# Performance work log

Hardware: AMD Instinct MI355X
Metric: run time of the kernel (lower is better)

## Reference

```python
import jax, jax.numpy as jnp
import numpy as np

B, T, D, HD = 8, 2048, 1024, 64

def setup_inputs() -> dict:
    key = jax.random.key(0)
    k1, k2, k3, k4 = jax.random.split(key, 4)
    x = jax.random.normal(k1, (B, T, D), dtype=jnp.float32)
    Wq = jax.random.normal(k2, (D, HD), dtype=jnp.float32) * (D ** -0.5)
    Wk = jax.random.normal(k3, (D, HD), dtype=jnp.float32) * (D ** -0.5)
    Wv = jax.random.normal(k4, (D, HD), dtype=jnp.float32) * (D ** -0.5)
    return {"x": x, "Wq": Wq, "Wk": Wk, "Wv": Wv}

def reference(x, Wq, Wk, Wv):
    # x: [B,T,D]; projections: [D,HD]
    q = jnp.einsum('btd,dh->bth', x, Wq)
    k = jnp.einsum('btd,dh->bth', x, Wk)
    v = jnp.einsum('btd,dh->bth', x, Wv)
    hd = q.shape[-1]
    scores = jnp.einsum('bth,bsh->bts', q, k) * (hd ** -0.5)  # [B,T,T]
    t = scores.shape[-1]
    causal = jnp.tril(jnp.ones((t, t), dtype=bool))
    scores = jnp.where(causal, scores, -jnp.inf)
    w = jax.nn.softmax(scores, axis=-1)
    # dropout p=0.0 (eval) -> identity
    return jnp.einsum('bts,bsh->bth', w, v)
```

## Files before the change

kernel.cpp:

```cpp
#include <hip/hip_runtime.h>
#include <hip/hip_bf16.h>
#include <stdint.h>

#define NB 8
#define TT 2048
#define DD 1024
#define HDIM 64

typedef __bf16 bf16x8 __attribute__((ext_vector_type(8)));
typedef float f32x4 __attribute__((ext_vector_type(4)));
typedef ushort u16x4 __attribute__((ext_vector_type(4)));

static_assert(sizeof(bf16x8) == 16, "bf16x8 must be 16 bytes");

__device__ inline ushort f2bf_bits(float f) {
    __hip_bfloat16 h = __float2bfloat16(f);
    return *reinterpret_cast<ushort*>(&h);
}
__device__ inline float bfbits2f(ushort u) {
    unsigned v = ((unsigned)u) << 16;
    return __builtin_bit_cast(float, v);
}
__device__ inline bf16x8 ldb8(const ushort* p) {
    return *reinterpret_cast<const bf16x8*>(p);
}

typedef __attribute__((address_space(3))) uint32_t lds_u32;
typedef const __attribute__((address_space(1))) uint32_t glb_u32;
__device__ inline void gl_lds16(const void* g, void* l) {
    __builtin_amdgcn_global_load_lds((glb_u32*)g, (lds_u32*)l, 16, 0, 0);
}

#define WCNT_VM2   0xF72
#define WCNT_VM5   0xF75
#define WCNT_LGKM0 0xC07F

__device__ inline int probe_f32(const ushort* x) {
    int lane = threadIdx.x & 63;
    int wild = 0;
    #pragma unroll
    for (int j = 0; j < 4; ++j) {
        ushort u = x[(lane * 4 + j) * 32];
        int e = (u >> 7) & 0xFF;
        wild += (e >= 0xC0);
    }
    unsigned long long m = __ballot(wild > 0);
    return __popcll(m) > 8;
}

__global__ __launch_bounds__(256) void k_wt(const ushort* __restrict__ x,
                                            const void* __restrict__ Wq,
                                            const void* __restrict__ Wk,
                                            const void* __restrict__ Wv,
                                            ushort* __restrict__ Wt) {
    int f32m = probe_f32(x);
    int idx = blockIdx.x * 256 + threadIdx.x;
    int mat = idx >> 16;
    int rem = idx & 65535;
    int d = rem >> 6;
    int h = rem & 63;
    const void* W = (mat == 0) ? Wq : (mat == 1) ? Wk : Wv;
    float v;
    if (f32m) v = ((const float*)W)[rem];
    else      v = bfbits2f(((const ushort*)W)[rem]);
    if (mat == 0) v *= 0.18033688011112042f;
    int n    = mat * 64 + h;
    int nt   = n >> 4, ncol = n & 15;
    int kk   = d >> 6, ks = (d >> 5) & 1, qd = (d >> 3) & 3, e = d & 7;
    int f    = nt * 2 + ks;
    Wt[((size_t)(kk * 24 + f)) * 512 + (qd * 16 + ncol) * 8 + e] = f2bf_bits(v);
}

template <int F32M>
__device__ inline void proj_body(const void* __restrict__ xv,
                                 const ushort* __restrict__ Wt,
                                 ushort* __restrict__ Qw,
                                 ushort* __restrict__ Kw,
                                 ushort* __restrict__ Vtw,
                                 ushort* Bf, ushort* Afb) {
    int tid  = threadIdx.x;
    int w    = tid >> 6;
    int lane = tid & 63;
    int quad = lane >> 4;
    int col  = lane & 15;
    int mtw  = w >> 2;
    int nh   = w & 3;
    int m0   = blockIdx.x * 64;

    const float*  xf = (const float*)xv;
    const ushort* xb = (const ushort*)xv;

    auto stageB = [&](int buf, int kkk) {
        int kk24 = (kkk >> 6) * 24;
        #pragma unroll
        for (int j = 0; j < 3; ++j) {
            int f = w * 3 + j;
            gl_lds16(Wt + ((size_t)(kk24 + f)) * 512 + lane * 8,
                     Bf + ((size_t)buf * 24 + f) * 512);
        }
    };

    int arow  = m0 + w * 8 + (lane >> 3);
    int amt_s = w >> 1;
    int colp  = (w & 1) * 8 + (lane >> 3);
    f32x4 arf[2];
    u16x4 arb[2];
    auto loadA = [&](int kkk) {
        #pragma unroll
        for (int i = 0; i < 2; ++i) {
            int c = (lane & 7) + i * 8;
            if (F32M) arf[i] = *reinterpret_cast<const f32x4*>(xf + (size_t)arow * DD + kkk + c * 4);
            else      arb[i] = *reinterpret_cast<const u16x4*>(xb + (size_t)arow * DD + kkk + c * 4);
        }
    };
    auto writeA = [&](int q) {
        #pragma unroll
        for (int i = 0; i < 2; ++i) {
            int c  = (lane & 7) + i * 8;
            int ks = i;
            int qd = (c & 7) >> 1;
            int e0 = (c & 1) * 4;
            u16x4 v;
            if (F32M) {
                #pragma unroll
                for (int j = 0; j < 4; ++j) v[j] = f2bf_bits(arf[i][j]);
            } else {
                v = arb[i];
            }
            *reinterpret_cast<u16x4*>(Afb + ((size_t)q * 16 + amt_s * 2 + ks) * 512
                                      + (qd * 16 + colp) * 8 + e0) = v;
        }
    };

    f32x4 acc[2][3];
    #pragma unroll
    for (int i = 0; i < 2; ++i)
        #pragma unroll
        for (int j = 0; j < 3; ++j) acc[i][j] = (f32x4){0.f, 0.f, 0.f, 0.f};

    loadA(0);
    stageB(0, 0);
    writeA(0);
    __builtin_amdgcn_s_waitcnt(WCNT_LGKM0);

    for (int t = 0; t < 16; ++t) {
        int p   = t & 1;
        int kn1 = (t + 1 < 16) ? (t + 1) * 64 : 960;
        loadA(kn1);
        stageB(p ^ 1, kn1);
        __builtin_amdgcn_s_waitcnt(WCNT_VM5);
        __builtin_amdgcn_s_barrier();

        #pragma unroll
        for (int ks = 0; ks < 2; ++ks) {
            bf16x8 a0 = ldb8(Afb + ((size_t)p * 16 + (mtw * 2 + 0) * 2 + ks) * 512 + lane * 8);
            bf16x8 a1 = ldb8(Afb + ((size_t)p * 16 + (mtw * 2 + 1) * 2 + ks) * 512 + lane * 8);
            #pragma unroll
            for (int j = 0; j < 3; ++j) {
                int nt = nh * 3 + j;
                bf16x8 b = ldb8(Bf + ((size_t)p * 24 + nt * 2 + ks) * 512 + lane * 8);
                acc[0][j] = __builtin_amdgcn_mfma_f32_16x16x32_bf16(a0, b, acc[0][j], 0, 0, 0);
                acc[1][j] = __builtin_amdgcn_mfma_f32_16x16x32_bf16(a1, b, acc[1][j], 0, 0, 0);
            }
        }
        writeA(p ^ 1);
        __builtin_amdgcn_s_waitcnt(WCNT_LGKM0);
        __builtin_amdgcn_s_barrier();
    }

    #pragma unroll
    for (int mloc = 0; mloc < 2; ++mloc) {
        #pragma unroll
        for (int j = 0; j < 3; ++j) {
            int nt  = nh * 3 + j;
            int mat = nt >> 2;
            int h   = (nt & 3) * 16 + col;
            if (mat == 2) {
                #pragma unroll
                for (int r = 0; r < 4; ++r) {
                    int row = m0 + mtw * 32 + mloc * 16 + quad * 4 + r;
                    int bb = row >> 11;
                    int t  = row & (TT - 1);
                    Vtw[(size_t)bb * HDIM * TT + (size_t)h * TT + t] = f2bf_bits(acc[mloc][j][r]);
                }
            } else {
                ushort* outp = (mat == 0) ? Qw : Kw;
                #pragma unroll
                for (int r = 0; r < 4; ++r) {
                    int row = m0 + mtw * 32 + mloc * 16 + quad * 4 + r;
                    outp[(size_t)row * HDIM + h] = f2bf_bits(acc[mloc][j][r]);
                }
            }
        }
    }
}

__global__ __launch_bounds__(512, 4) void k_proj(const void* __restrict__ xv,
                                                 const ushort* __restrict__ Wt,
                                                 ushort* __restrict__ Qw,
                                                 ushort* __restrict__ Kw,
                                                 ushort* __restrict__ Vtw) {
    __shared__ ushort Bf[2 * 24 * 512];
    __shared__ ushort Afb[2 * 16 * 512];
    if (probe_f32((const ushort*)xv)) proj_body<1>(xv, Wt, Qw, Kw, Vtw, Bf, Afb);
    else                              proj_body<0>(xv, Wt, Qw, Kw, Vtw, Bf, Afb);
}

__global__ __launch_bounds__(256) void k_attn(const ushort* __restrict__ Qw,
                                              const ushort* __restrict__ Kw,
                                              const ushort* __restrict__ Vtw,
                                              ushort* __restrict__ Po,
                                              float* __restrict__ Pl) {
    int w    = threadIdx.x >> 6;
    int lane = threadIdx.x & 63;
    int quad = lane >> 4;
    int col  = lane & 15;
    int bid  = blockIdx.x;
    int b    = bid & 7;
    int idx  = 79 - (bid >> 3);
    int c, g;
    if (idx < 32)      { c = 0; g = idx; }
    else if (idx < 56) { c = 1; g = idx - 24; }
    else if (idx < 72) { c = 2; g = idx - 40; }
    else               { c = 3; g = idx - 48; }
    int qb = 4 * g + w;
    int m0 = qb * 16;
    int Bq = (qb < 32) ? qb : (qb < 64) ? 2*qb - 32 : (qb < 96) ? 3*qb - 96 : 4*qb - 192;
    int pid = b * 320 + Bq + c;

    const ushort* Qb = Qw + (size_t)b * TT * HDIM;
    const ushort* Kb = Kw + (size_t)b * TT * HDIM;
    const ushort* Vb = Vtw + (size_t)b * HDIM * TT;

    __shared__ ushort KVb[2][8][512];
    __shared__ __hip_bfloat16 Pls[4][16][40];

    auto stageKV = [&](int buf, int s) {
        #pragma unroll
        for (int j = 0; j < 2; ++j) {
            int f = w * 2 + j;
            const ushort* gp;
            if (f < 4) {
                int half = f & 1;
                int ro   = (f >> 1) * 16;
                gp = Kb + (size_t)(s + ro + col) * HDIM + half * 32 + quad * 8;
            } else {
                int vg = f - 4;
                gp = Vb + (size_t)(vg * 16 + col) * TT + s + quad * 8;
            }
            gl_lds16(gp, &KVb[buf][f][0]);
        }
    };

    bf16x8 qf0 = ldb8(Qb + (size_t)(m0 + col) * HDIM + quad * 8);
    bf16x8 qf1 = ldb8(Qb + (size_t)(m0 + col) * HDIM + 32 + quad * 8);

    f32x4 o0 = {0.f,0.f,0.f,0.f};
    f32x4 o1 = {0.f,0.f,0.f,0.f};
    f32x4 o2 = {0.f,0.f,0.f,0.f};
    f32x4 o3 = {0.f,0.f,0.f,0.f};
    float rsum[4] = {0.f, 0.f, 0.f, 0.f};

    const int start = c * 512;
    const int end   = min(start + 512, 64 * g + 64);

    stageKV(0, start);
    for (int s0 = start; s0 < end; s0 += 32) {
        int p  = ((s0 - start) >> 5) & 1;
        int sn = (s0 + 32 < end) ? s0 + 32 : s0;
        stageKV(p ^ 1, sn);
        __builtin_amdgcn_s_waitcnt(WCNT_VM2);
        __builtin_amdgcn_s_barrier();

        if (s0 < m0 + 16) {
            bf16x8 ck0l = ldb8(&KVb[p][0][lane * 8]);
            bf16x8 ck0h = ldb8(&KVb[p][1][lane * 8]);
            bf16x8 ck1l = ldb8(&KVb[p][2][lane * 8]);
            bf16x8 ck1h = ldb8(&KVb[p][3][lane * 8]);

            f32x4 S0 = {0.f,0.f,0.f,0.f};
            f32x4 S1 = {0.f,0.f,0.f,0.f};
            S0 = __builtin_amdgcn_mfma_f32_16x16x32_bf16(qf0, ck0l, S0, 0, 0, 0);
            S0 = __builtin_amdgcn_mfma_f32_16x16x32_bf16(qf1, ck0h, S0, 0, 0, 0);
            S1 = __builtin_amdgcn_mfma_f32_16x16x32_bf16(qf0, ck1l, S1, 0, 0, 0);
            S1 = __builtin_amdgcn_mfma_f32_16x16x32_bf16(qf1, ck1h, S1, 0, 0, 0);

            #pragma unroll
            for (int r = 0; r < 4; ++r) {
                int trow = m0 + quad * 4 + r;
                float aa = (s0 + col      > trow) ? -1e30f : S0[r];
                float dd = (s0 + 16 + col > trow) ? -1e30f : S1[r];
                float p0 = exp2f(aa);
                float p1 = exp2f(dd);
                rsum[r] += p0 + p1;
                Pls[w][quad * 4 + r][col]      = __float2bfloat16(p0);
                Pls[w][quad * 4 + r][16 + col] = __float2bfloat16(p1);
            }
            bf16x8 pf = *reinterpret_cast<const bf16x8*>(&Pls[w][col][quad * 8]);

            bf16x8 cv0 = ldb8(&KVb[p][4][lane * 8]);
            bf16x8 cv1 = ldb8(&KVb[p][5][lane * 8]);
            bf16x8 cv2 = ldb8(&KVb[p][6][lane * 8]);
            bf16x8 cv3 = ldb8(&KVb[p][7][lane * 8]);
            o0 = __builtin_amdgcn_mfma_f32_16x16x32_bf16(pf, cv0, o0, 0, 0, 0);
            o1 = __builtin_amdgcn_mfma_f32_16x16x32_bf16(pf, cv1, o1, 0, 0, 0);
            o2 = __builtin_amdgcn_mfma_f32_16x16x32_bf16(pf, cv2, o2, 0, 0, 0);
            o3 = __builtin_amdgcn_mfma_f32_16x16x32_bf16(pf, cv3, o3, 0, 0, 0);
        }
        __builtin_amdgcn_s_waitcnt(WCNT_LGKM0);
        __builtin_amdgcn_s_barrier();
    }

    #pragma unroll
    for (int off = 1; off < 16; off <<= 1) {
        #pragma unroll
        for (int r = 0; r < 4; ++r)
            rsum[r] += __shfl_xor(rsum[r], off, 64);
    }

    ushort* pb = Po + (size_t)pid * 1024;
    #pragma unroll
    for (int r = 0; r < 4; ++r) {
        int row = quad * 4 + r;
        pb[row * 64 + 0*16 + col] = f2bf_bits(o0[r]);
        pb[row * 64 + 1*16 + col] = f2bf_bits(o1[r]);
        pb[row * 64 + 2*16 + col] = f2bf_bits(o2[r]);
        pb[row * 64 + 3*16 + col] = f2bf_bits(o3[r]);
        if (col == 0) Pl[pid * 16 + row] = rsum[r];
    }
}

__global__ __launch_bounds__(256) void k_merge(const ushort* __restrict__ x,
                                               const ushort* __restrict__ Po,
                                               const float* __restrict__ Pl,
                                               void* __restrict__ outv) {
    int f32m = probe_f32(x);
    int wid  = blockIdx.x * 4 + (threadIdx.x >> 6);
    int lane = threadIdx.x & 63;
    int row  = lane >> 2;
    int g    = lane & 3;
    int b    = wid >> 7;
    int qb   = wid & 127;
    int nch  = (qb >> 5) + 1;
    int Bq   = (qb < 32) ? qb : (qb < 64) ? 2*qb - 32 : (qb < 96) ? 3*qb - 96 : 4*qb - 192;
    int pid0 = b * 320 + Bq;

    float L = 0.f;
    #pragma unroll
    for (int c = 0; c < 4; ++c)
        if (c < nch) L += Pl[(pid0 + c) * 16 + row];
    float inv = 1.0f / L;

    float o[16];
    #pragma unroll
    for (int j = 0; j < 16; ++j) o[j] = 0.f;
    #pragma unroll
    for (int c = 0; c < 4; ++c) {
        if (c < nch) {
            const ushort* p = Po + (size_t)(pid0 + c) * 1024 + row * 64 + g * 16;
            bf16x8 v0 = ldb8(p);
            bf16x8 v1 = ldb8(p + 8);
            #pragma unroll
            for (int j = 0; j < 8; ++j) {
                o[j]     += (float)v0[j];
                o[8 + j] += (float)v1[j];
            }
        }
    }

    size_t obase = ((size_t)b * TT + qb * 16 + row) * HDIM + g * 16;
    if (f32m) {
        float* ob = (float*)outv + obase;
        #pragma unroll
        for (int j = 0; j < 16; ++j) ob[j] = o[j] * inv;
    } else {
        ushort* ob = (ushort*)outv + obase;
        #pragma unroll
        for (int j = 0; j < 16; ++j) ob[j] = f2bf_bits(o[j] * inv);
    }
}

extern "C" void kernel_launch(void* const* d_in, const int* in_sizes, int n_in,
                              void* d_out, int out_size, void* d_ws, size_t ws_size,
                              hipStream_t stream) {
    const ushort* x = (const ushort*)d_in[0];
    ushort* Wt  = (ushort*)d_ws;
    ushort* Qw  = Wt + 3 * HDIM * DD;
    ushort* Kw  = Qw + (size_t)NB * TT * HDIM;
    ushort* Vtw = Kw + (size_t)NB * TT * HDIM;
    ushort* Po  = Vtw + (size_t)NB * TT * HDIM;
    float*  Pl  = (float*)(Po + (size_t)2560 * 1024);

    k_wt   <<<768, 256, 0, stream>>>(x, d_in[1], d_in[2], d_in[3], Wt);
    k_proj <<<256, 512, 0, stream>>>(d_in[0], Wt, Qw, Kw, Vtw);
    k_attn <<<640, 256, 0, stream>>>(Qw, Kw, Vtw, Po, Pl);
    k_merge<<<256, 256, 0, stream>>>(x, Po, Pl, d_out);
}
```

Baseline: 144.7 us.

## Transpose attention MFMAs to keep P in registers via shuffles instead of LDS

Swaps the MFMA operand order so S and O are computed transposed (keys/head-dim along rows, queries along lanes). P is then repacked into the B-operand layout with cross-lane shuffles, which removes the per-iteration LDS round-trip through the Pls scratch buffer. Each lane now owns a single query row, so the row sum needs only two shuffle steps. Partial outputs are written as 8-byte vector stores. In exchange it adds eight shuffles plus selects per iteration and relies on the transposed layout matching the merge kernel's expectations.

```diff
diff --git a/kernel.cpp b/kernel.cpp
--- a/kernel.cpp
+++ b/kernel.cpp
@@ -10,6 +10,7 @@
 typedef __bf16 bf16x8 __attribute__((ext_vector_type(8)));
 typedef float f32x4 __attribute__((ext_vector_type(4)));
 typedef ushort u16x4 __attribute__((ext_vector_type(4)));
+typedef unsigned int u32x4 __attribute__((ext_vector_type(4)));
 
 static_assert(sizeof(bf16x8) == 16, "bf16x8 must be 16 bytes");
 
@@ -233,7 +234,6 @@
     const ushort* Vb = Vtw + (size_t)b * HDIM * TT;
 
     __shared__ ushort KVb[2][8][512];
-    __shared__ __hip_bfloat16 Pls[4][16][40];
 
     auto stageKV = [&](int buf, int s) {
         #pragma unroll
@@ -259,10 +259,13 @@
     f32x4 o1 = {0.f,0.f,0.f,0.f};
     f32x4 o2 = {0.f,0.f,0.f,0.f};
     f32x4 o3 = {0.f,0.f,0.f,0.f};
-    float rsum[4] = {0.f, 0.f, 0.f, 0.f};
+    float rsum = 0.f;
 
     const int start = c * 512;
     const int end   = min(start + 512, 64 * g + 64);
+    const int qrow  = m0 + col;
+    const int hi    = quad >> 1;
+    const int lowsrc = ((quad & 1) << 5) + col;
 
     stageKV(0, start);
     for (int s0 = start; s0 < end; s0 += 32) {
@@ -280,54 +283,68 @@
 
             f32x4 S0 = {0.f,0.f,0.f,0.f};
             f32x4 S1 = {0.f,0.f,0.f,0.f};
-            S0 = __builtin_amdgcn_mfma_f32_16x16x32_bf16(qf0, ck0l, S0, 0, 0, 0);
-            S0 = __builtin_amdgcn_mfma_f32_16x16x32_bf16(qf1, ck0h, S0, 0, 0, 0);
-            S1 = __builtin_amdgcn_mfma_f32_16x16x32_bf16(qf0, ck1l, S1, 0, 0, 0);
-            S1 = __builtin_amdgcn_mfma_f32_16x16x32_bf16(qf1, ck1h, S1, 0, 0, 0);
-
+            S0 = __builtin_amdgcn_mfma_f32_16x16x32_bf16(ck0l, qf0, S0, 0, 0, 0);
+            S0 = __builtin_amdgcn_mfma_f32_16x16x32_bf16(ck0h, qf1, S0, 0, 0, 0);
+            S1 = __builtin_amdgcn_mfma_f32_16x16x32_bf16(ck1l, qf0, S1, 0, 0, 0);
+            S1 = __builtin_amdgcn_mfma_f32_16x16x32_bf16(ck1h, qf1, S1, 0, 0, 0);
+
+            int kb0 = s0 + quad * 4;
+            float p0[4], p1[4];
             #pragma unroll
             for (int r = 0; r < 4; ++r) {
-                int trow = m0 + quad * 4 + r;
-                float aa = (s0 + col      > trow) ? -1e30f : S0[r];
-                float dd = (s0 + 16 + col > trow) ? -1e30f : S1[r];
-                float p0 = exp2f(aa);
-                float p1 = exp2f(dd);
-                rsum[r] += p0 + p1;
-                Pls[w][quad * 4 + r][col]      = __float2bfloat16(p0);
-                Pls[w][quad * 4 + r][16 + col] = __float2bfloat16(p1);
-            }
-            bf16x8 pf = *reinterpret_cast<const bf16x8*>(&Pls[w][col][quad * 8]);
+                p0[r] = exp2f((kb0 + r      > qrow) ? -1e30f : S0[r]);
+                p1[r] = exp2f((kb0 + 16 + r > qrow) ? -1e30f : S1[r]);
+                rsum += p0[r] + p1[r];
+            }
+            unsigned A0 = (unsigned)f2bf_bits(p0[0]) | ((unsigned)f2bf_bits(p0[1]) << 16);
+            unsigned A1 = (unsigned)f2bf_bits(p0[2]) | ((unsigned)f2bf_bits(p0[3]) << 16);
+            unsigned B0 = (unsigned)f2bf_bits(p1[0]) | ((unsigned)f2bf_bits(p1[1]) << 16);
+            unsigned B1 = (unsigned)f2bf_bits(p1[2]) | ((unsigned)f2bf_bits(p1[3]) << 16);
+
+            int t0, u0;
+            t0 = __shfl((int)A0, lowsrc, 64);      u0 = __shfl((int)B0, lowsrc, 64);
+            unsigned w0 = hi ? (unsigned)u0 : (unsigned)t0;
+            t0 = __shfl((int)A1, lowsrc, 64);      u0 = __shfl((int)B1, lowsrc, 64);
+            unsigned w1 = hi ? (unsigned)u0 : (unsigned)t0;
+            t0 = __shfl((int)A0, lowsrc + 16, 64); u0 = __shfl((int)B0, lowsrc + 16, 64);
+            unsigned w2 = hi ? (unsigned)u0 : (unsigned)t0;
+            t0 = __shfl((int)A1, lowsrc + 16, 64); u0 = __shfl((int)B1, lowsrc + 16, 64);
+            unsigned w3 = hi ? (unsigned)u0 : (unsigned)t0;
+            bf16x8 pf = __builtin_bit_cast(bf16x8, (u32x4){w0, w1, w2, w3});
 
             bf16x8 cv0 = ldb8(&KVb[p][4][lane * 8]);
             bf16x8 cv1 = ldb8(&KVb[p][5][lane * 8]);
             bf16x8 cv2 = ldb8(&KVb[p][6][lane * 8]);
             bf16x8 cv3 = ldb8(&KVb[p][7][lane * 8]);
-            o0 = __builtin_amdgcn_mfma_f32_16x16x32_bf16(pf, cv0, o0, 0, 0, 0);
-            o1 = __builtin_amdgcn_mfma_f32_16x16x32_bf16(pf, cv1, o1, 0, 0, 0);
-            o2 = __builtin_amdgcn_mfma_f32_16x16x32_bf16(pf, cv2, o2, 0, 0, 0);
-            o3 = __builtin_amdgcn_mfma_f32_16x16x32_bf16(pf, cv3, o3, 0, 0, 0);
+            o0 = __builtin_amdgcn_mfma_f32_16x16x32_bf16(cv0, pf, o0, 0, 0, 0);
+            o1 = __builtin_amdgcn_mfma_f32_16x16x32_bf16(cv1, pf, o1, 0, 0, 0);
+            o2 = __builtin_amdgcn_mfma_f32_16x16x32_bf16(cv2, pf, o2, 0, 0, 0);
+            o3 = __builtin_amdgcn_mfma_f32_16x16x32_bf16(cv3, pf, o3, 0, 0, 0);
         }
         __builtin_amdgcn_s_waitcnt(WCNT_LGKM0);
         __builtin_amdgcn_s_barrier();
     }
 
-    #pragma unroll
-    for (int off = 1; off < 16; off <<= 1) {
-        #pragma unroll
-        for (int r = 0; r < 4; ++r)
-            rsum[r] += __shfl_xor(rsum[r], off, 64);
-    }
+    rsum += __shfl_xor(rsum, 16, 64);
+    rsum += __shfl_xor(rsum, 32, 64);
 
     ushort* pb = Po + (size_t)pid * 1024;
-    #pragma unroll
-    for (int r = 0; r < 4; ++r) {
-        int row = quad * 4 + r;
-        pb[row * 64 + 0*16 + col] = f2bf_bits(o0[r]);
-        pb[row * 64 + 1*16 + col] = f2bf_bits(o1[r]);
-        pb[row * 64 + 2*16 + col] = f2bf_bits(o2[r]);
-        pb[row * 64 + 3*16 + col] = f2bf_bits(o3[r]);
-        if (col == 0) Pl[pid * 16 + row] = rsum[r];
-    }
+    {
+        u16x4 v;
+        #pragma unroll
+        for (int r = 0; r < 4; ++r) v[r] = f2bf_bits(o0[r]);
+        *reinterpret_cast<u16x4*>(pb + col * 64 + 0 * 16 + quad * 4) = v;
+        #pragma unroll
+        for (int r = 0; r < 4; ++r) v[r] = f2bf_bits(o1[r]);
+        *reinterpret_cast<u16x4*>(pb + col * 64 + 1 * 16 + quad * 4) = v;
+        #pragma unroll
+        for (int r = 0; r < 4; ++r) v[r] = f2bf_bits(o2[r]);
+        *reinterpret_cast<u16x4*>(pb + col * 64 + 2 * 16 + quad * 4) = v;
+        #pragma unroll
+        for (int r = 0; r < 4; ++r) v[r] = f2bf_bits(o3[r]);
+        *reinterpret_cast<u16x4*>(pb + col * 64 + 3 * 16 + quad * 4) = v;
+    }
+    if (quad == 0) Pl[pid * 16 + col] = rsum;
 }
 
 __global__ __launch_bounds__(256) void k_merge(const ushort* __restrict__ x,
```

Result: no change. 146.8 us (+1.5%).

## Tile V transpose into 32-key blocks and swizzle K/V staging for coalescing

Applied to the files above, without the earlier changes.

The projection kernel now stores V transposed in per-32-key tiles (each tile holding 64 dims by 32 keys contiguously) and writes four consecutive keys per lane as one vector store. The attention kernel stages K and V with fully contiguous row loads into LDS using an XOR swizzle, and reads MFMA fragments through matching swizzled slot functions. The goal is to replace the strided 16-byte global accesses of the old V-transposed layout with contiguous ones and to avoid LDS bank conflicts. The swizzle index math is intricate, so any mismatch between the staging and read mappings would produce wrong results.

```diff
diff --git a/kernel.cpp b/kernel.cpp
--- a/kernel.cpp
+++ b/kernel.cpp
@@ -76,7 +76,7 @@
                                  const ushort* __restrict__ Wt,
                                  ushort* __restrict__ Qw,
                                  ushort* __restrict__ Kw,
-                                 ushort* __restrict__ Vtw,
+                                 ushort* __restrict__ V2,
                                  ushort* Bf, ushort* Afb) {
     int tid  = threadIdx.x;
     int w    = tid >> 6;
@@ -176,13 +176,15 @@
             int mat = nt >> 2;
             int h   = (nt & 3) * 16 + col;
             if (mat == 2) {
+                int row0 = m0 + mtw * 32 + mloc * 16 + quad * 4;
+                int bb   = row0 >> 11;
+                int t0   = row0 & (TT - 1);
+                u16x4 v;
                 #pragma unroll
-                for (int r = 0; r < 4; ++r) {
-                    int row = m0 + mtw * 32 + mloc * 16 + quad * 4 + r;
-                    int bb = row >> 11;
-                    int t  = row & (TT - 1);
-                    Vtw[(size_t)bb * HDIM * TT + (size_t)h * TT + t] = f2bf_bits(acc[mloc][j][r]);
-                }
+                for (int r = 0; r < 4; ++r) v[r] = f2bf_bits(acc[mloc][j][r]);
+                *reinterpret_cast<u16x4*>(V2 + (size_t)bb * HDIM * TT
+                                          + (size_t)(t0 >> 5) * 2048
+                                          + h * 32 + (t0 & 31)) = v;
             } else {
                 ushort* outp = (mat == 0) ? Qw : Kw;
                 #pragma unroll
@@ -199,16 +201,16 @@
                                                  const ushort* __restrict__ Wt,
                                                  ushort* __restrict__ Qw,
                                                  ushort* __restrict__ Kw,
-                                                 ushort* __restrict__ Vtw) {
+                                                 ushort* __restrict__ V2) {
     __shared__ ushort Bf[2 * 24 * 512];
     __shared__ ushort Afb[2 * 16 * 512];
-    if (probe_f32((const ushort*)xv)) proj_body<1>(xv, Wt, Qw, Kw, Vtw, Bf, Afb);
-    else                              proj_body<0>(xv, Wt, Qw, Kw, Vtw, Bf, Afb);
+    if (probe_f32((const ushort*)xv)) proj_body<1>(xv, Wt, Qw, Kw, V2, Bf, Afb);
+    else                              proj_body<0>(xv, Wt, Qw, Kw, V2, Bf, Afb);
 }
 
 __global__ __launch_bounds__(256) void k_attn(const ushort* __restrict__ Qw,
                                               const ushort* __restrict__ Kw,
-                                              const ushort* __restrict__ Vtw,
+                                              const ushort* __restrict__ V2w,
                                               ushort* __restrict__ Po,
                                               float* __restrict__ Pl) {
     int w    = threadIdx.x >> 6;
@@ -228,28 +230,39 @@
     int Bq = (qb < 32) ? qb : (qb < 64) ? 2*qb - 32 : (qb < 96) ? 3*qb - 96 : 4*qb - 192;
     int pid = b * 320 + Bq + c;
 
-    const ushort* Qb = Qw + (size_t)b * TT * HDIM;
-    const ushort* Kb = Kw + (size_t)b * TT * HDIM;
-    const ushort* Vb = Vtw + (size_t)b * HDIM * TT;
-
-    __shared__ ushort KVb[2][8][512];
+    const ushort* Qb  = Qw  + (size_t)b * TT * HDIM;
+    const ushort* Kb  = Kw  + (size_t)b * TT * HDIM;
+    const ushort* V2b = V2w + (size_t)b * HDIM * TT;
+
+    __shared__ ushort KVb[2][4096];
     __shared__ __hip_bfloat16 Pls[4][16][40];
 
     auto stageKV = [&](int buf, int s) {
         #pragma unroll
         for (int j = 0; j < 2; ++j) {
-            int f = w * 2 + j;
+            int i = w * 2 + j;
             const ushort* gp;
-            if (f < 4) {
-                int half = f & 1;
-                int ro   = (f >> 1) * 16;
-                gp = Kb + (size_t)(s + ro + col) * HDIM + half * 32 + quad * 8;
+            if (i < 4) {
+                int row = i * 8 + (lane >> 3);
+                int cg  = (lane & 7) ^ (lane >> 3);
+                gp = Kb + (size_t)(s + row) * HDIM + cg * 8;
             } else {
-                int vg = f - 4;
-                gp = Vb + (size_t)(vg * 16 + col) * TT + s + quad * 8;
-            }
-            gl_lds16(gp, &KVb[buf][f][0]);
-        }
+                int w3 = (lane & 7) ^ (lane >> 3);
+                int d  = (i - 4) * 16 + 2 * (lane >> 3) + (w3 >> 2);
+                int cg = w3 & 3;
+                gp = V2b + (size_t)(s >> 5) * 2048 + d * 32 + cg * 8;
+            }
+            gl_lds16(gp, &KVb[buf][i * 512]);
+        }
+    };
+
+    int cb7  = col & 7;
+    int vlow = (quad + 4 * (col & 1)) ^ ((col >> 1) & 7);
+    auto kslot = [&](int rb, int half) {
+        return ((rb + col) * 8 + ((half * 4 + quad) ^ cb7)) * 8;
+    };
+    auto vslot = [&](int vg) {
+        return 2048 + ((vg * 8 + (col >> 1)) * 8 + vlow) * 8;
     };
 
     bf16x8 qf0 = ldb8(Qb + (size_t)(m0 + col) * HDIM + quad * 8);
@@ -273,10 +286,10 @@
         __builtin_amdgcn_s_barrier();
 
         if (s0 < m0 + 16) {
-            bf16x8 ck0l = ldb8(&KVb[p][0][lane * 8]);
-            bf16x8 ck0h = ldb8(&KVb[p][1][lane * 8]);
-            bf16x8 ck1l = ldb8(&KVb[p][2][lane * 8]);
-            bf16x8 ck1h = ldb8(&KVb[p][3][lane * 8]);
+            bf16x8 ck0l = ldb8(&KVb[p][kslot(0,  0)]);
+            bf16x8 ck0h = ldb8(&KVb[p][kslot(0,  1)]);
+            bf16x8 ck1l = ldb8(&KVb[p][kslot(16, 0)]);
+            bf16x8 ck1h = ldb8(&KVb[p][kslot(16, 1)]);
 
             f32x4 S0 = {0.f,0.f,0.f,0.f};
             f32x4 S1 = {0.f,0.f,0.f,0.f};
@@ -298,10 +311,10 @@
             }
             bf16x8 pf = *reinterpret_cast<const bf16x8*>(&Pls[w][col][quad * 8]);
 
-            bf16x8 cv0 = ldb8(&KVb[p][4][lane * 8]);
-            bf16x8 cv1 = ldb8(&KVb[p][5][lane * 8]);
-            bf16x8 cv2 = ldb8(&KVb[p][6][lane * 8]);
-            bf16x8 cv3 = ldb8(&KVb[p][7][lane * 8]);
+            bf16x8 cv0 = ldb8(&KVb[p][vslot(0)]);
+            bf16x8 cv1 = ldb8(&KVb[p][vslot(1)]);
+            bf16x8 cv2 = ldb8(&KVb[p][vslot(2)]);
+            bf16x8 cv3 = ldb8(&KVb[p][vslot(3)]);
             o0 = __builtin_amdgcn_mfma_f32_16x16x32_bf16(pf, cv0, o0, 0, 0, 0);
             o1 = __builtin_amdgcn_mfma_f32_16x16x32_bf16(pf, cv1, o1, 0, 0, 0);
             o2 = __builtin_amdgcn_mfma_f32_16x16x32_bf16(pf, cv2, o2, 0, 0, 0);
@@ -387,12 +400,12 @@
     ushort* Wt  = (ushort*)d_ws;
     ushort* Qw  = Wt + 3 * HDIM * DD;
     ushort* Kw  = Qw + (size_t)NB * TT * HDIM;
-    ushort* Vtw = Kw + (size_t)NB * TT * HDIM;
-    ushort* Po  = Vtw + (size_t)NB * TT * HDIM;
+    ushort* V2  = Kw + (size_t)NB * TT * HDIM;
+    ushort* Po  = V2 + (size_t)NB * TT * HDIM;
     float*  Pl  = (float*)(Po + (size_t)2560 * 1024);
 
     k_wt   <<<768, 256, 0, stream>>>(x, d_in[1], d_in[2], d_in[3], Wt);
-    k_proj <<<256, 512, 0, stream>>>(d_in[0], Wt, Qw, Kw, Vtw);
-    k_attn <<<640, 256, 0, stream>>>(Qw, Kw, Vtw, Po, Pl);
+    k_proj <<<256, 512, 0, stream>>>(d_in[0], Wt, Qw, Kw, V2);
+    k_attn <<<640, 256, 0, stream>>>(Qw, Kw, V2, Po, Pl);
     k_merge<<<256, 256, 0, stream>>>(x, Po, Pl, d_out);
 }
```

After: 142.4 us, median of 2. Within noise of the previous version (-1.6%).
